# Performance work log

Measured on AMD Instinct MI355X. Metric: run time of the kernel, lower is better.

Reference implementation:

```python
import jax, jax.numpy as jnp
import numpy as np

HEADS = 16

def setup_inputs() -> dict:
    key = jax.random.key(0)
    ks = jax.random.split(key, 12)
    S, E = 2048, 1024
    x = jax.random.normal(ks[0], (S, E), dtype=jnp.float32)
    seg = jnp.sort(jax.random.randint(ks[1], (S,), 0, 32)).astype(jnp.int32)
    sc = 1.0 / np.sqrt(E)
    Wq = jax.random.normal(ks[2], (E, E), dtype=jnp.float32) * sc
    bq = jax.random.normal(ks[3], (E,), dtype=jnp.float32) * 0.01
    Wk = jax.random.normal(ks[4], (E, E), dtype=jnp.float32) * sc
    bk = jax.random.normal(ks[5], (E,), dtype=jnp.float32) * 0.01
    Wv = jax.random.normal(ks[6], (E, E), dtype=jnp.float32) * sc
    bv = jax.random.normal(ks[7], (E,), dtype=jnp.float32) * 0.01
    Wo = jax.random.normal(ks[8], (E, E), dtype=jnp.float32) * sc
    bo = jax.random.normal(ks[9], (E,), dtype=jnp.float32) * 0.01
    return {"x": x, "seg": seg, "pos": 1000,
            "Wq": Wq, "bq": bq, "Wk": Wk, "bk": bk,
            "Wv": Wv, "bv": bv, "Wo": Wo, "bo": bo}

def reference(x, seg, pos, Wq, bq, Wk, bk, Wv, bv, Wo, bo):
    S, E = x.shape
    H = HEADS
    d = E // H
    # projections: [S,E] -> [H,S,d]
    q = (x @ Wq + bq).reshape(S, H, d).transpose(1, 0, 2)
    k = (x @ Wk + bk).reshape(S, H, d).transpose(1, 0, 2)
    v = (x @ Wv + bv).reshape(S, H, d).transpose(1, 0, 2)
    # raw scores (note: original code applies NO 1/sqrt(d) scaling)
    scores = jnp.einsum('hid,hjd->hij', q, k)  # [H,S,S]
    same_seg = seg[:, None] == seg[None, :]    # [S,S]
    # faithful to original: out-of-segment entries stay ZERO (not -inf)
    scores = jnp.where(same_seg[None, :, :], scores, 0.0)
    weights = jax.nn.softmax(scores, axis=-1)
    out = jnp.einsum('hij,hjd->hid', weights, v)          # [H,S,d]
    out = out.transpose(1, 0, 2).reshape(S, E)            # [S,E]
    result = out @ Wo + bo                                # [S,E]
    # mean over the segment containing `pos`
    m = (seg == seg[pos]).astype(result.dtype)            # [S]
    return (result * m[:, None]).sum(axis=0) / m.sum()
```

## Files before the change

### kernel.cpp

```cpp
#include <hip/hip_runtime.h>

#define SS 2048
#define EE 1024
#define NH 16
#define DH 64
#define NR 128


__device__ __forceinline__ int rfl(int v) {
    return __builtin_amdgcn_readfirstlane(v);
}

__device__ __forceinline__ int2 seg_bounds(const int* __restrict__ seg,
                                           const int* __restrict__ pos) {
    __shared__ int sb[8];
    int t = threadIdx.x;
    int g = seg[pos[0]];
    int lomin = SS, himax = 0;
    const int4* s4 = (const int4*)seg;
#pragma unroll
    for (int i = t; i < SS / 4; i += 256) {
        int4 v = s4[i];
        int b = i * 4;
        if (v.x == g) { lomin = min(lomin, b);     himax = max(himax, b + 1); }
        if (v.y == g) { lomin = min(lomin, b + 1); himax = max(himax, b + 2); }
        if (v.z == g) { lomin = min(lomin, b + 2); himax = max(himax, b + 3); }
        if (v.w == g) { lomin = min(lomin, b + 3); himax = max(himax, b + 4); }
    }
    for (int o = 32; o; o >>= 1) {
        lomin = min(lomin, __shfl_xor(lomin, o, 64));
        himax = max(himax, __shfl_xor(himax, o, 64));
    }
    if ((t & 63) == 0) { sb[t >> 6] = lomin; sb[4 + (t >> 6)] = himax; }
    __syncthreads();
    return make_int2(min(min(sb[0], sb[1]), min(sb[2], sb[3])),
                     max(max(sb[4], sb[5]), max(sb[6], sb[7])));
}

__global__ void __launch_bounds__(256, 4) k_d1(
    const float* __restrict__ x, const int* __restrict__ seg,
    const int* __restrict__ pos,
    const float* __restrict__ Wq, const float* __restrict__ bq,
    const float* __restrict__ Wk, const float* __restrict__ bk,
    const float* __restrict__ Wv, const float* __restrict__ bv,
    float* __restrict__ xsum, int* __restrict__ meta,
    float* __restrict__ Q, float* __restrict__ K, float* __restrict__ V,
    int nmax) {
    __shared__ float red[1024];
    const int t = threadIdx.x, wv = t >> 6, lane = t & 63;

    if (blockIdx.z == 0) {
        int xb = blockIdx.y * 16 + blockIdx.x;
        if (xb < 64) {
            const float4* x4 = (const float4*)x + (size_t)(xb * 32) * 256 + t;
            float4 a = make_float4(0.f, 0.f, 0.f, 0.f);
#pragma unroll 8
            for (int r = 0; r < 32; ++r) {
                float4 v = x4[(size_t)r * 256];
                a.x += v.x; a.y += v.y; a.z += v.z; a.w += v.w;
            }
            int e0 = 4 * t;
            atomicAdd(&xsum[e0 + 0], a.x);
            atomicAdd(&xsum[e0 + 1], a.y);
            atomicAdd(&xsum[e0 + 2], a.z);
            atomicAdd(&xsum[e0 + 3], a.w);
        } else if (xb == 64) {
            int2 bnd = seg_bounds(seg, pos);
            if (t == 0) { meta[0] = bnd.x; meta[1] = bnd.y; }
        }
        return;
    }

    int2 bnd = seg_bounds(seg, pos);
    int lo = bnd.x;
    int nc = bnd.y - lo; if (nc > nmax) nc = nmax; if (nc < 1) nc = 1;
    int mat = blockIdx.z - 1;
    const float* W  = mat == 0 ? Wq : mat == 1 ? Wk : Wv;
    const float* bb = mat == 0 ? bq : mat == 1 ? bk : bv;
    float* dst      = mat == 0 ? Q  : mat == 1 ? K  : V;
    int e = blockIdx.x * 64 + lane;
    int kbu = rfl(wv) * 256;
    const float* Wp = W + (size_t)kbu * EE + e;
    float bias = bb[e];

    for (int rt = blockIdx.y; rt * 4 < nc; rt += 16) {
        int r0 = rt * 4;
        int rB = min(r0 + 1, nc - 1);
        int rC = min(r0 + 2, nc - 1);
        int rD = min(r0 + 3, nc - 1);
        const float* xA = x + (size_t)rfl(lo + r0) * EE + kbu;
        const float* xB = x + (size_t)rfl(lo + rB) * EE + kbu;
        const float* xC = x + (size_t)rfl(lo + rC) * EE + kbu;
        const float* xD = x + (size_t)rfl(lo + rD) * EE + kbu;
        float a0 = 0.f, a1 = 0.f, a2 = 0.f, a3 = 0.f;
#pragma unroll 8
        for (int c = 0; c < 256; ++c) {
            float wj = Wp[(size_t)c * EE];
            a0 += xA[c] * wj;
            a1 += xB[c] * wj;
            a2 += xC[c] * wj;
            a3 += xD[c] * wj;
        }
        __syncthreads();
        red[(wv * 4 + 0) * 64 + lane] = a0;
        red[(wv * 4 + 1) * 64 + lane] = a1;
        red[(wv * 4 + 2) * 64 + lane] = a2;
        red[(wv * 4 + 3) * 64 + lane] = a3;
        __syncthreads();
        float s = red[(0 * 4 + wv) * 64 + lane] + red[(1 * 4 + wv) * 64 + lane]
                + red[(2 * 4 + wv) * 64 + lane] + red[(3 * 4 + wv) * 64 + lane]
                + bias;
        int gr = r0 + wv;
        if (gr < nc)
            dst[(size_t)gr * EE + e] = s;
    }
}

__global__ void __launch_bounds__(256, 4) k_d2(
    const float* __restrict__ Wv, const float* __restrict__ bv,
    const float* __restrict__ xsum, const int* __restrict__ meta,
    const float* __restrict__ Q, const float* __restrict__ K,
    const float* __restrict__ V,
    float* __restrict__ vtot, float* __restrict__ A, float* __restrict__ Bh,
    int nmax) {
    __shared__ float lds[2048];
    const int t = threadIdx.x, wv = t >> 6, lane = t & 63;
    const int bid = blockIdx.x, gb = gridDim.x;

    if (bid < 16) {
        ((float4*)lds)[t] = ((const float4*)xsum)[t];
        __syncthreads();
        int e = bid * 64 + lane;
        int kbu = rfl(wv) * 256;
        const float* Wp = Wv + (size_t)kbu * EE + e;
        const float4* xs4 = (const float4*)(lds + kbu);
        float a = 0.f;
#pragma unroll 4
        for (int c = 0; c < 256; c += 4) {
            float4 xv = xs4[c >> 2];
            a += xv.x * Wp[(size_t)(c + 0) * EE]
               + xv.y * Wp[(size_t)(c + 1) * EE]
               + xv.z * Wp[(size_t)(c + 2) * EE]
               + xv.w * Wp[(size_t)(c + 3) * EE];
        }
        __syncthreads();
        lds[1024 + wv * 64 + lane] = a;
        __syncthreads();
        if (wv == 0) {
            float s = lds[1024 + lane] + lds[1088 + lane]
                    + lds[1152 + lane] + lds[1216 + lane];
            vtot[e] = s + bv[e] * (float)SS;
        }
        return;
    }

    int lo = meta[0];
    int nc = meta[1] - lo; if (nc > nmax) nc = nmax; if (nc < 1) nc = 1;
    int nit = nc * NH;
    float* ql = lds + wv * 512;
    float* sb = ql + 64;
    for (int it = (bid - 16) * 4 + wv; it < nit; it += (gb - 16) * 4) {
        int r = it >> 4, h = it & 15;
        ql[lane] = Q[(size_t)r * EE + h * DH + lane];
        asm volatile("s_waitcnt lgkmcnt(0)" ::: "memory");
        const float4* q4 = (const float4*)ql;
        float m = 0.f;
        for (int j = lane; j < nc; j += 64) {
            const float4* kr = (const float4*)(K + (size_t)j * EE + h * DH);
            float s = 0.f;
#pragma unroll 4
            for (int d = 0; d < DH / 4; ++d) {
                float4 kv = kr[d];
                float4 qv = q4[d];
                s += qv.x * kv.x + qv.y * kv.y + qv.z * kv.z + qv.w * kv.w;
            }
            sb[j] = s;
            m = fmaxf(m, s);
        }
        for (int o = 32; o; o >>= 1) m = fmaxf(m, __shfl_xor(m, o, 64));
        float dl = 0.f;
        for (int j = lane; j < nc; j += 64) {
            float wgt = __expf(sb[j] - m);
            sb[j] = wgt;
            dl += wgt;
        }
        for (int o = 32; o; o >>= 1) dl += __shfl_xor(dl, o, 64);
        float em = __expf(-m);
        float denom = dl + (float)(SS - nc) * em;
        asm volatile("s_waitcnt lgkmcnt(0)" ::: "memory");
        float acc = 0.f, vs = 0.f;
        const float* Vp = V + h * DH + lane;
        int j = 0;
        for (; j + 4 <= nc; j += 4) {
            float4 wq = *(const float4*)(sb + j);
            float v0 = Vp[(size_t)(j + 0) * EE];
            float v1 = Vp[(size_t)(j + 1) * EE];
            float v2 = Vp[(size_t)(j + 2) * EE];
            float v3 = Vp[(size_t)(j + 3) * EE];
            acc += wq.x * v0 + wq.y * v1 + wq.z * v2 + wq.w * v3;
            vs  += v0 + v1 + v2 + v3;
        }
        for (; j < nc; ++j) {
            float v0 = Vp[(size_t)j * EE];
            acc += sb[j] * v0;
            vs  += v0;
        }
        atomicAdd(&A[h * DH + lane], (acc - vs * em) / denom);
        if (lane == 0) atomicAdd(&Bh[h], em / denom);
    }
}

__global__ void __launch_bounds__(256, 4) k_d3(
    const int* __restrict__ meta,
    const float* __restrict__ Wo, const float* __restrict__ bo,
    const float* __restrict__ vtot, const float* __restrict__ A,
    const float* __restrict__ Bh, int nmax, float* __restrict__ out) {
    __shared__ float lds[1344];
    const int t = threadIdx.x, wv = t >> 6, lane = t & 63;
    int nc = meta[1] - meta[0]; if (nc > nmax) nc = nmax; if (nc < 1) nc = 1;
    {
        float4 av = ((const float4*)A)[t];
        float4 vv = ((const float4*)vtot)[t];
        float bh = Bh[t >> 4];
        float4 o4;
        o4.x = av.x + vv.x * bh;
        o4.y = av.y + vv.y * bh;
        o4.z = av.z + vv.z * bh;
        o4.w = av.w + vv.w * bh;
        ((float4*)lds)[t] = o4;
    }
    __syncthreads();
    int e = blockIdx.x * 64 + lane;
    int kbu = rfl(wv) * 256;
    const float* Wp = Wo + (size_t)kbu * EE + e;
    const float4* os4 = (const float4*)(lds + kbu);
    float a = 0.f;
#pragma unroll 4
    for (int c = 0; c < 256; c += 4) {
        float4 ov = os4[c >> 2];
        a += ov.x * Wp[(size_t)(c + 0) * EE]
           + ov.y * Wp[(size_t)(c + 1) * EE]
           + ov.z * Wp[(size_t)(c + 2) * EE]
           + ov.w * Wp[(size_t)(c + 3) * EE];
    }
    __syncthreads();
    lds[1024 + wv * 64 + lane] = a;
    __syncthreads();
    if (wv == 0) {
        float s = lds[1024 + lane] + lds[1088 + lane]
                + lds[1152 + lane] + lds[1216 + lane];
        out[e] = bo[e] + s / (float)nc;
    }
}

extern "C" void kernel_launch(void* const* d_in, const int* in_sizes, int n_in,
                              void* d_out, int out_size, void* d_ws, size_t ws_size,
                              hipStream_t stream) {
    const float* x  = (const float*)d_in[0];
    const int* seg  = (const int*)d_in[1];
    const int* pos  = (const int*)d_in[2];
    const float* Wq = (const float*)d_in[3];
    const float* bq = (const float*)d_in[4];
    const float* Wk = (const float*)d_in[5];
    const float* bk = (const float*)d_in[6];
    const float* Wv = (const float*)d_in[7];
    const float* bv = (const float*)d_in[8];
    const float* Wo = (const float*)d_in[9];
    const float* bo = (const float*)d_in[10];
    float* out = (float*)d_out;

    char* w = (char*)d_ws;
    float* xsum = (float*)(w + 0);
    float* A    = (float*)(w + 4096);
    float* Bh   = (float*)(w + 8192);
    int*   meta = (int*)(w + 8256);
    float* vtot = (float*)(w + 12288);

    size_t base = 16384;
    size_t avail = (ws_size > base) ? ws_size - base : 0;
    int nmax = (int)(avail / (3ull * EE * sizeof(float)));
    if (nmax > NR) nmax = NR;
    if (nmax < 1) nmax = 1;
    float* Q = (float*)(w + base);
    float* K = Q + (size_t)nmax * EE;
    float* V = K + (size_t)nmax * EE;

    hipMemsetAsync(w, 0, 8264, stream);
    k_d1<<<dim3(16, 16, 4), 256, 0, stream>>>(
        x, seg, pos, Wq, bq, Wk, bk, Wv, bv, xsum, meta, Q, K, V, nmax);
    k_d2<<<272, 256, 0, stream>>>(
        Wv, bv, xsum, meta, Q, K, V, vtot, A, Bh, nmax);
    k_d3<<<16, 256, 0, stream>>>(meta, Wo, bo, vtot, A, Bh, nmax, out);
}
```

Before: 157.6 us.

## Widen blocks to 1024 threads, replace memset and atomics with partial sums

k_d1 and k_d3 now run with 1024-thread blocks, splitting the K reduction across 16 waves that each cover 64 columns instead of 4 waves covering 256. The x column sum no longer uses atomics into a memset buffer. Each block writes per-row-group partial sums, and k_d2 reduces the 64 partials. Zeroing of A and Bh moves into k_d1, so the hipMemsetAsync launch is dropped. This removes a launch and the atomic contention and adds parallelism to the small GEMV kernels, at the cost of larger LDS reductions and more barrier overhead per block.

```diff
diff --git a/kernel.cpp b/kernel.cpp
--- a/kernel.cpp
+++ b/kernel.cpp
@@ -13,13 +13,12 @@
 
 __device__ __forceinline__ int2 seg_bounds(const int* __restrict__ seg,
                                            const int* __restrict__ pos) {
-    __shared__ int sb[8];
-    int t = threadIdx.x;
+    __shared__ int sb[32];
+    int t = threadIdx.x, nthr = blockDim.x;
     int g = seg[pos[0]];
     int lomin = SS, himax = 0;
     const int4* s4 = (const int4*)seg;
-#pragma unroll
-    for (int i = t; i < SS / 4; i += 256) {
+    for (int i = t; i < SS / 4; i += nthr) {
         int4 v = s4[i];
         int b = i * 4;
         if (v.x == g) { lomin = min(lomin, b);     himax = max(himax, b + 1); }
@@ -31,40 +30,46 @@
         lomin = min(lomin, __shfl_xor(lomin, o, 64));
         himax = max(himax, __shfl_xor(himax, o, 64));
     }
-    if ((t & 63) == 0) { sb[t >> 6] = lomin; sb[4 + (t >> 6)] = himax; }
+    if ((t & 63) == 0) { sb[t >> 6] = lomin; sb[16 + (t >> 6)] = himax; }
     __syncthreads();
-    return make_int2(min(min(sb[0], sb[1]), min(sb[2], sb[3])),
-                     max(max(sb[4], sb[5]), max(sb[6], sb[7])));
-}
-
-__global__ void __launch_bounds__(256, 4) k_d1(
+    int nw = nthr >> 6;
+    lomin = SS; himax = 0;
+    for (int wq = 0; wq < nw; ++wq) {
+        lomin = min(lomin, sb[wq]);
+        himax = max(himax, sb[16 + wq]);
+    }
+    return make_int2(lomin, himax);
+}
+
+__global__ void __launch_bounds__(1024, 4) k_d1(
     const float* __restrict__ x, const int* __restrict__ seg,
     const int* __restrict__ pos,
     const float* __restrict__ Wq, const float* __restrict__ bq,
     const float* __restrict__ Wk, const float* __restrict__ bk,
     const float* __restrict__ Wv, const float* __restrict__ bv,
-    float* __restrict__ xsum, int* __restrict__ meta,
+    float* __restrict__ xpart, int* __restrict__ meta,
+    float* __restrict__ A, float* __restrict__ Bh,
     float* __restrict__ Q, float* __restrict__ K, float* __restrict__ V,
     int nmax) {
-    __shared__ float red[1024];
+    __shared__ float red[4096];
     const int t = threadIdx.x, wv = t >> 6, lane = t & 63;
 
     if (blockIdx.z == 0) {
-        int xb = blockIdx.y * 16 + blockIdx.x;
-        if (xb < 64) {
-            const float4* x4 = (const float4*)x + (size_t)(xb * 32) * 256 + t;
+        if (blockIdx.y == 0) {
+            int xb = blockIdx.x;
+            int col4 = t & 255, rgrp = t >> 8;
+            const float4* x4 = (const float4*)x
+                + (size_t)(xb * 128 + rgrp * 32) * 256 + col4;
             float4 a = make_float4(0.f, 0.f, 0.f, 0.f);
 #pragma unroll 8
             for (int r = 0; r < 32; ++r) {
                 float4 v = x4[(size_t)r * 256];
                 a.x += v.x; a.y += v.y; a.z += v.z; a.w += v.w;
             }
-            int e0 = 4 * t;
-            atomicAdd(&xsum[e0 + 0], a.x);
-            atomicAdd(&xsum[e0 + 1], a.y);
-            atomicAdd(&xsum[e0 + 2], a.z);
-            atomicAdd(&xsum[e0 + 3], a.w);
-        } else if (xb == 64) {
+            ((float4*)(xpart + (size_t)(xb * 4 + rgrp) * EE))[col4] = a;
+        } else if (blockIdx.y == 1 && blockIdx.x == 0) {
+            A[t] = 0.f;
+            if (t < 16) Bh[t] = 0.f;
             int2 bnd = seg_bounds(seg, pos);
             if (t == 0) { meta[0] = bnd.x; meta[1] = bnd.y; }
         }
@@ -79,9 +84,8 @@
     const float* bb = mat == 0 ? bq : mat == 1 ? bk : bv;
     float* dst      = mat == 0 ? Q  : mat == 1 ? K  : V;
     int e = blockIdx.x * 64 + lane;
-    int kbu = rfl(wv) * 256;
+    int kbu = rfl(wv) * 64;
     const float* Wp = W + (size_t)kbu * EE + e;
-    float bias = bb[e];
 
     for (int rt = blockIdx.y; rt * 4 < nc; rt += 16) {
         int r0 = rt * 4;
@@ -94,7 +98,7 @@
         const float* xD = x + (size_t)rfl(lo + rD) * EE + kbu;
         float a0 = 0.f, a1 = 0.f, a2 = 0.f, a3 = 0.f;
 #pragma unroll 8
-        for (int c = 0; c < 256; ++c) {
+        for (int c = 0; c < 64; ++c) {
             float wj = Wp[(size_t)c * EE];
             a0 += xA[c] * wj;
             a1 += xB[c] * wj;
@@ -102,23 +106,28 @@
             a3 += xD[c] * wj;
         }
         __syncthreads();
-        red[(wv * 4 + 0) * 64 + lane] = a0;
-        red[(wv * 4 + 1) * 64 + lane] = a1;
-        red[(wv * 4 + 2) * 64 + lane] = a2;
-        red[(wv * 4 + 3) * 64 + lane] = a3;
-        __syncthreads();
-        float s = red[(0 * 4 + wv) * 64 + lane] + red[(1 * 4 + wv) * 64 + lane]
-                + red[(2 * 4 + wv) * 64 + lane] + red[(3 * 4 + wv) * 64 + lane]
-                + bias;
-        int gr = r0 + wv;
-        if (gr < nc)
-            dst[(size_t)gr * EE + e] = s;
+        red[((wv << 2) + 0) * 64 + lane] = a0;
+        red[((wv << 2) + 1) * 64 + lane] = a1;
+        red[((wv << 2) + 2) * 64 + lane] = a2;
+        red[((wv << 2) + 3) * 64 + lane] = a3;
+        __syncthreads();
+        if (t < 256) {
+            int row = t >> 6, col = t & 63;
+            float s = 0.f;
+#pragma unroll
+            for (int w = 0; w < 16; ++w)
+                s += red[((w << 2) + row) * 64 + col];
+            s += bb[blockIdx.x * 64 + col];
+            int gr = r0 + row;
+            if (gr < nc)
+                dst[(size_t)gr * EE + blockIdx.x * 64 + col] = s;
+        }
     }
 }
 
 __global__ void __launch_bounds__(256, 4) k_d2(
     const float* __restrict__ Wv, const float* __restrict__ bv,
-    const float* __restrict__ xsum, const int* __restrict__ meta,
+    const float* __restrict__ xpart, const int* __restrict__ meta,
     const float* __restrict__ Q, const float* __restrict__ K,
     const float* __restrict__ V,
     float* __restrict__ vtot, float* __restrict__ A, float* __restrict__ Bh,
@@ -128,23 +137,30 @@
     const int bid = blockIdx.x, gb = gridDim.x;
 
     if (bid < 16) {
-        ((float4*)lds)[t] = ((const float4*)xsum)[t];
+        float4 a = make_float4(0.f, 0.f, 0.f, 0.f);
+        const float4* xp4 = (const float4*)xpart + t;
+#pragma unroll 8
+        for (int b = 0; b < 64; ++b) {
+            float4 v = xp4[(size_t)b * 256];
+            a.x += v.x; a.y += v.y; a.z += v.z; a.w += v.w;
+        }
+        ((float4*)lds)[t] = a;
         __syncthreads();
         int e = bid * 64 + lane;
         int kbu = rfl(wv) * 256;
         const float* Wp = Wv + (size_t)kbu * EE + e;
         const float4* xs4 = (const float4*)(lds + kbu);
-        float a = 0.f;
+        float acc = 0.f;
 #pragma unroll 4
         for (int c = 0; c < 256; c += 4) {
             float4 xv = xs4[c >> 2];
-            a += xv.x * Wp[(size_t)(c + 0) * EE]
-               + xv.y * Wp[(size_t)(c + 1) * EE]
-               + xv.z * Wp[(size_t)(c + 2) * EE]
-               + xv.w * Wp[(size_t)(c + 3) * EE];
-        }
-        __syncthreads();
-        lds[1024 + wv * 64 + lane] = a;
+            acc += xv.x * Wp[(size_t)(c + 0) * EE]
+                 + xv.y * Wp[(size_t)(c + 1) * EE]
+                 + xv.z * Wp[(size_t)(c + 2) * EE]
+                 + xv.w * Wp[(size_t)(c + 3) * EE];
+        }
+        __syncthreads();
+        lds[1024 + wv * 64 + lane] = acc;
         __syncthreads();
         if (wv == 0) {
             float s = lds[1024 + lane] + lds[1088 + lane]
@@ -210,46 +226,31 @@
     }
 }
 
-__global__ void __launch_bounds__(256, 4) k_d3(
+__global__ void __launch_bounds__(1024, 4) k_d3(
     const int* __restrict__ meta,
     const float* __restrict__ Wo, const float* __restrict__ bo,
     const float* __restrict__ vtot, const float* __restrict__ A,
     const float* __restrict__ Bh, int nmax, float* __restrict__ out) {
-    __shared__ float lds[1344];
+    __shared__ float lds[2048];
     const int t = threadIdx.x, wv = t >> 6, lane = t & 63;
     int nc = meta[1] - meta[0]; if (nc > nmax) nc = nmax; if (nc < 1) nc = 1;
-    {
-        float4 av = ((const float4*)A)[t];
-        float4 vv = ((const float4*)vtot)[t];
-        float bh = Bh[t >> 4];
-        float4 o4;
-        o4.x = av.x + vv.x * bh;
-        o4.y = av.y + vv.y * bh;
-        o4.z = av.z + vv.z * bh;
-        o4.w = av.w + vv.w * bh;
-        ((float4*)lds)[t] = o4;
-    }
+    lds[t] = A[t] + vtot[t] * Bh[t >> 6];
     __syncthreads();
     int e = blockIdx.x * 64 + lane;
-    int kbu = rfl(wv) * 256;
+    int kbu = rfl(wv) * 64;
     const float* Wp = Wo + (size_t)kbu * EE + e;
-    const float4* os4 = (const float4*)(lds + kbu);
     float a = 0.f;
-#pragma unroll 4
-    for (int c = 0; c < 256; c += 4) {
-        float4 ov = os4[c >> 2];
-        a += ov.x * Wp[(size_t)(c + 0) * EE]
-           + ov.y * Wp[(size_t)(c + 1) * EE]
-           + ov.z * Wp[(size_t)(c + 2) * EE]
-           + ov.w * Wp[(size_t)(c + 3) * EE];
-    }
-    __syncthreads();
+#pragma unroll 8
+    for (int c = 0; c < 64; ++c)
+        a += lds[kbu + c] * Wp[(size_t)c * EE];
     lds[1024 + wv * 64 + lane] = a;
     __syncthreads();
-    if (wv == 0) {
-        float s = lds[1024 + lane] + lds[1088 + lane]
-                + lds[1152 + lane] + lds[1216 + lane];
-        out[e] = bo[e] + s / (float)nc;
+    if (t < 64) {
+        float s = 0.f;
+#pragma unroll
+        for (int w = 0; w < 16; ++w)
+            s += lds[1024 + w * 64 + t];
+        out[blockIdx.x * 64 + t] = bo[blockIdx.x * 64 + t] + s / (float)nc;
     }
 }
 
@@ -270,13 +271,13 @@
     float* out = (float*)d_out;
 
     char* w = (char*)d_ws;
-    float* xsum = (float*)(w + 0);
-    float* A    = (float*)(w + 4096);
-    float* Bh   = (float*)(w + 8192);
-    int*   meta = (int*)(w + 8256);
-    float* vtot = (float*)(w + 12288);
-
-    size_t base = 16384;
+    float* A     = (float*)(w + 0);
+    float* Bh    = (float*)(w + 4096);
+    int*   meta  = (int*)(w + 4160);
+    float* vtot  = (float*)(w + 8192);
+    float* xpart = (float*)(w + 16384);
+
+    size_t base = 16384 + 64 * EE * sizeof(float);
     size_t avail = (ws_size > base) ? ws_size - base : 0;
     int nmax = (int)(avail / (3ull * EE * sizeof(float)));
     if (nmax > NR) nmax = NR;
@@ -285,10 +286,9 @@
     float* K = Q + (size_t)nmax * EE;
     float* V = K + (size_t)nmax * EE;
 
-    hipMemsetAsync(w, 0, 8264, stream);
-    k_d1<<<dim3(16, 16, 4), 256, 0, stream>>>(
-        x, seg, pos, Wq, bq, Wk, bk, Wv, bv, xsum, meta, Q, K, V, nmax);
+    k_d1<<<dim3(16, 16, 4), 1024, 0, stream>>>(
+        x, seg, pos, Wq, bq, Wk, bk, Wv, bv, xpart, meta, A, Bh, Q, K, V, nmax);
     k_d2<<<272, 256, 0, stream>>>(
-        Wv, bv, xsum, meta, Q, K, V, vtot, A, Bh, nmax);
-    k_d3<<<16, 256, 0, stream>>>(meta, Wo, bo, vtot, A, Bh, nmax, out);
-}
+        Wv, bv, xpart, meta, Q, K, V, vtot, A, Bh, nmax);
+    k_d3<<<16, 1024, 0, stream>>>(meta, Wo, bo, vtot, A, Bh, nmax, out);
+}
```

Measured after the change: 137.8 us. -12.6%, faster.
